# Performance work log

Hardware: AMD Instinct MI355X
Metric: run time of the kernel (lower is better)

The kernel has to match this reference:

```python
import jax, jax.numpy as jnp
import numpy as np
from jax import lax

THRESHOLD = 10.0


def _conv(x, w):
    # x: [N,1,H,W], w: [O,1,kh,kw], SAME padding, stride 1 (matches nn.Conv2d with symmetric padding)
    return lax.conv_general_dilated(x, w, window_strides=(1, 1), padding='SAME',
                                    dimension_numbers=('NCHW', 'OIHW', 'NCHW'))


def _make_filters():
    # scipy.signal.gaussian(5, std=1.0): unnormalized gaussian window
    gauss = np.exp(-0.5 * ((np.arange(5) - 2.0) ** 2)).astype(np.float32)
    gauss_w = gauss.reshape(1, 1, 1, 5)  # horizontal 1x5 filter
    sobel = np.array([[1, 0, -1], [2, 0, -2], [1, 0, -1]], np.float32)
    sobel_x = sobel[None, None]  # [1,1,3,3]
    f0 = [[0, 0, 0], [0, 1, -1], [0, 0, 0]]
    f45 = [[0, 0, 0], [0, 1, 0], [0, 0, -1]]
    f90 = [[0, 0, 0], [0, 1, 0], [0, -1, 0]]
    f135 = [[0, 0, 0], [0, 1, 0], [-1, 0, 0]]
    f180 = [[0, 0, 0], [-1, 1, 0], [0, 0, 0]]
    f225 = [[-1, 0, 0], [0, 1, 0], [0, 0, 0]]
    f270 = [[0, -1, 0], [0, 1, 0], [0, 0, 0]]
    f315 = [[0, 0, -1], [0, 1, 0], [0, 0, 0]]
    dir_w = np.stack([f0, f45, f90, f135, f180, f225, f270, f315]).astype(np.float32)[:, None]  # [8,1,3,3]
    return jnp.asarray(gauss_w), jnp.asarray(sobel_x), jnp.asarray(dir_w)


def setup_inputs() -> dict:
    key = jax.random.key(0)
    B, H, W = 4, 1024, 1024
    img = jax.random.uniform(key, (B, 3, H, W), dtype=jnp.float32) * 255.0  # pixel-scale values
    gauss_w, sobel_x, dir_w = _make_filters()
    return {'img': img, 'gauss_w': gauss_w, 'sobel_x': sobel_x, 'dir_w': dir_w}


def reference(img, gauss_w, sobel_x, dir_w):
    B, C, H, W = img.shape  # C == 3
    x = img.reshape(B * 3, 1, H, W)
    # Separable gaussian blur (horizontal then vertical), all 3 channels batched together
    blurred = _conv(_conv(x, gauss_w), jnp.transpose(gauss_w, (0, 1, 3, 2)))  # [B*3,1,H,W]
    # Sobel gradients per channel
    gx = _conv(blurred, sobel_x).reshape(B, 3, H, W)
    gy = _conv(blurred, jnp.transpose(sobel_x, (0, 1, 3, 2))).reshape(B, 3, H, W)
    # Magnitude: sum of per-channel L2 magnitudes
    grad_mag = jnp.sum(jnp.sqrt(gx * gx + gy * gy), axis=1, keepdims=True)  # [B,1,H,W]
    # Orientation from summed gradients, quantized to 45-degree bins (same pi constant as original)
    grad_orientation = jnp.arctan2(gy.sum(1, keepdims=True), gx.sum(1, keepdims=True)) * (180.0 / 3.14159)
    grad_orientation = jnp.round((grad_orientation + 180.0) / 45.0) * 45.0
    # Directional differences for non-max suppression
    all_filtered = _conv(grad_mag, dir_w)  # [B,8,H,W]
    idx_pos = ((grad_orientation / 45.0) % 8).astype(jnp.int32)          # [B,1,H,W]
    idx_neg = ((grad_orientation / 45.0 + 4.0) % 8).astype(jnp.int32)
    pos = jnp.take_along_axis(all_filtered, idx_pos, axis=1)  # [B,1,H,W]
    neg = jnp.take_along_axis(all_filtered, idx_neg, axis=1)
    is_max = jnp.minimum(pos, neg) > 0.0
    thin_edges = jnp.where(is_max, grad_mag, 0.0)
    thresholded = jnp.where(thin_edges < THRESHOLD, 0.0, thin_edges)
    early_threshold = jnp.where(grad_mag < THRESHOLD, 0.0, grad_mag)
    blurred_img = blurred.reshape(B, 3, H, W)[None]  # matches torch.stack([squeeze(...)]) for B>1
    return (blurred_img, grad_mag, grad_orientation, thin_edges, thresholded, early_threshold)
```

## Files before the change

### kernel.cpp

```cpp
#include <hip/hip_runtime.h>
#include <math.h>

#define TILE 32
#define RAW  40
#define RS   44
#define VB   36
#define MG   34
#define NT   256

struct TrigC { double c0, s0, c1, s1, c2, s2, c3, s3; };

__global__ __launch_bounds__(NT, 4) void canny_fused_kernel(
    const float* __restrict__ img,
    const float* __restrict__ gauss,
    float* __restrict__ out_blur,
    float* __restrict__ out_mag,
    float* __restrict__ out_ori,
    float* __restrict__ out_thin,
    float* __restrict__ out_thr,
    float* __restrict__ out_early,
    TrigC tc, int H, int W)
{
    __shared__ double s_raw[RAW * RS];
    __shared__ double s_vb [VB * VB];
    __shared__ double s_mag[MG * MG];

    const int tid = threadIdx.x;
    const int b   = blockIdx.z;
    const int gy0 = blockIdx.y * TILE;
    const int gx0 = blockIdx.x * TILE;
    const bool interior = (gy0 >= 4) && (gy0 + 36 <= H) && (gx0 >= 8) && (gx0 + 36 <= W);

    const double g0 = (double)gauss[0], g1 = (double)gauss[1], g2 = (double)gauss[2];
    const size_t cs = (size_t)H * W;

    for (int i = tid; i < MG * MG; i += NT) s_mag[i] = 0.0;

    double agx0 = 0.0, agx1 = 0.0, agx2 = 0.0, agx3 = 0.0;
    double agy0 = 0.0, agy1 = 0.0, agy2 = 0.0, agy3 = 0.0;

    auto load_raw = [&](int c) {
        const float* ip = img + (size_t)(b * 3 + c) * cs;
        if (interior) {
            const float* rowbase = ip + (size_t)(gy0 - 4) * W + (gx0 - 8);
            for (int t = tid; t < RAW * 11; t += NT) {
                int ry = t / 11, rx = t - ry * 11;
                float4 v = *reinterpret_cast<const float4*>(rowbase + (size_t)ry * W + rx * 4);
                double* d = &s_raw[ry * RS + rx * 4];
                d[0] = (double)v.x; d[1] = (double)v.y;
                d[2] = (double)v.z; d[3] = (double)v.w;
            }
        } else {
            for (int t = tid; t < RAW * RAW; t += NT) {
                int ry = t / RAW, rx = t - ry * RAW;
                int y = gy0 + ry - 4, x = gx0 + rx - 4;
                float v = 0.f;
                if ((unsigned)y < (unsigned)H && (unsigned)x < (unsigned)W)
                    v = ip[(size_t)y * W + x];
                s_raw[ry * RS + rx + 4] = (double)v;
            }
        }
    };

    load_raw(0);
    __syncthreads();

    for (int c = 0; c < 3; ++c) {
        if (tid < 216) {
            const int xi    = tid % 36;
            const int y0    = (tid / 36) * 6;
            const double* rb = &s_raw[xi + 4];
            auto hrow = [&](int r) -> double {
                const double* p = rb + r * RS;
                return g0 * (p[0] + p[4]) + g1 * (p[1] + p[3]) + g2 * p[2];
            };
            double h0 = hrow(y0), h1 = hrow(y0 + 1), h2 = hrow(y0 + 2),
                   h3 = hrow(y0 + 3), h4 = hrow(y0 + 4);
#pragma unroll
            for (int t = 0; t < 6; ++t) {
                int yi = y0 + t;
                double acc = g0 * (h0 + h4) + g1 * (h1 + h3) + g2 * h2;
                if (!interior) {
                    int y = gy0 + yi - 2, x = gx0 + xi - 2;
                    if ((unsigned)y >= (unsigned)H || (unsigned)x >= (unsigned)W) acc = 0.0;
                }
                s_vb[yi * VB + xi] = acc;
                if (t < 5) { h0 = h1; h1 = h2; h2 = h3; h3 = h4; h4 = hrow(yi + 5); }
            }
        }
        __syncthreads();

        {
            int ry = tid >> 5, rx = tid & 31;
#pragma unroll 4
            for (int p = 0; p < 4; ++p) {
                int my = ry + 8 * p + 1, mx = rx + 1;
                const double* v = s_vb + my * VB + mx;
                double a00 = v[0],      a01 = v[1],          a02 = v[2];
                double a10 = v[VB],                          a12 = v[VB + 2];
                double a20 = v[2 * VB], a21 = v[2 * VB + 1], a22 = v[2 * VB + 2];
                double gx = (a00 - a02) + 2.0 * (a10 - a12) + (a20 - a22);
                double gy = (a00 - a20) + 2.0 * (a01 - a21) + (a02 - a22);
                s_mag[my * MG + mx] += sqrt(gx * gx + gy * gy);
                if (p == 0) { agx0 += gx; agy0 += gy; }
                else if (p == 1) { agx1 += gx; agy1 += gy; }
                else if (p == 2) { agx2 += gx; agy2 += gy; }
                else { agx3 += gx; agy3 += gy; }
            }
        }
        if (tid < 132) {
            int my, mx;
            if (tid < 34)       { my = 0;            mx = tid; }
            else if (tid < 68)  { my = 33;           mx = tid - 34; }
            else if (tid < 100) { my = tid - 68 + 1; mx = 0; }
            else                { my = tid - 100 + 1; mx = 33; }
            bool inimg = interior;
            if (!interior) {
                int y = gy0 + my - 1, x = gx0 + mx - 1;
                inimg = ((unsigned)y < (unsigned)H) && ((unsigned)x < (unsigned)W);
            }
            if (inimg) {
                const double* v = s_vb + my * VB + mx;
                double a00 = v[0],      a01 = v[1],          a02 = v[2];
                double a10 = v[VB],                          a12 = v[VB + 2];
                double a20 = v[2 * VB], a21 = v[2 * VB + 1], a22 = v[2 * VB + 2];
                double gx = (a00 - a02) + 2.0 * (a10 - a12) + (a20 - a22);
                double gy = (a00 - a20) + 2.0 * (a01 - a21) + (a02 - a22);
                s_mag[my * MG + mx] += sqrt(gx * gx + gy * gy);
            }
        }
        {
            float* bp = out_blur + (size_t)(b * 3 + c) * cs;
            int ry = tid >> 5, rx = tid & 31;
#pragma unroll 4
            for (int p = 0; p < 4; ++p)
                bp[(size_t)(gy0 + ry + 8 * p) * W + (gx0 + rx)] =
                    (float)s_vb[(ry + 8 * p + 2) * VB + (rx + 2)];
        }
        if (c < 2) load_raw(c + 1);
        __syncthreads();
    }

    const size_t ob = (size_t)b * cs;
#pragma unroll 4
    for (int p = 0; p < 4; ++p) {
        int i = tid + p * NT;
        int ry = i >> 5, rx = i & 31;
        double gxv = (p == 0) ? agx0 : (p == 1) ? agx1 : (p == 2) ? agx2 : agx3;
        double gyv = (p == 0) ? agy0 : (p == 1) ? agy1 : (p == 2) ? agy2 : agy3;
        double m = s_mag[(ry + 1) * MG + (rx + 1)];

        double a = fabs(gyv);
        int n = (int)(a * tc.c0 - gxv * tc.s0 >= 0.0)
              + (int)(a * tc.c1 - gxv * tc.s1 >= 0.0)
              + (int)(a * tc.c2 - gxv * tc.s2 >= 0.0)
              + (int)(a * tc.c3 - gxv * tc.s3 >= 0.0);
        int k;
        if (gyv == 0.0) {
            bool gxneg = signbit(gxv);
            k = signbit(gyv) ? (gxneg ? 0 : 4) : (gxneg ? 8 : 4);
        } else {
            k = signbit(gyv) ? 4 - n : 4 + n;
        }
        float q = 45.f * (float)k;
        if (gxv < 0.0 && fabs(gyv) < 1e-2) q = 180.f;

        int kp = k & 7;
        int dy = (int)((0x00012221u >> (kp * 4)) & 7u) - 1;
        int dx = (int)((0x21000122u >> (kp * 4)) & 7u) - 1;
        double pos = m - s_mag[(ry + 1 + dy) * MG + (rx + 1 + dx)];
        double neg = m - s_mag[(ry + 1 - dy) * MG + (rx + 1 - dx)];
        float mf = (float)m;
        float thin = (fmin(pos, neg) > 0.0) ? mf : 0.f;
        size_t idx = ob + (size_t)(gy0 + ry) * W + (gx0 + rx);
        out_mag[idx]   = mf;
        out_ori[idx]   = q;
        out_thin[idx]  = thin;
        out_thr[idx]   = (thin < 10.f) ? 0.f : thin;
        out_early[idx] = (mf < 10.f) ? 0.f : mf;
    }
}

extern "C" void kernel_launch(void* const* d_in, const int* in_sizes, int n_in,
                              void* d_out, int out_size, void* d_ws, size_t ws_size,
                              hipStream_t stream) {
    const float* img   = (const float*)d_in[0];
    const float* gauss = (const float*)d_in[1];
    const int H = 1024, W = 1024;
    const int B = in_sizes[0] / (3 * H * W);

    float* out = (float*)d_out;
    const size_t cs = (size_t)H * W;
    float* out_blur  = out;
    float* out_mag   = out_blur + (size_t)B * 3 * cs;
    float* out_ori   = out_mag  + (size_t)B * cs;
    float* out_thin  = out_ori  + (size_t)B * cs;
    float* out_thr   = out_thin + (size_t)B * cs;
    float* out_early = out_thr  + (size_t)B * cs;

    const double C = 180.0 / 3.14159;
    TrigC tc;
    { double bta = 22.5 / C;  tc.c0 = cos(bta); tc.s0 = sin(bta); }
    { double bta = 67.5 / C;  tc.c1 = cos(bta); tc.s1 = sin(bta); }
    { double bta = 112.5 / C; tc.c2 = cos(bta); tc.s2 = sin(bta); }
    { double bta = 157.5 / C; tc.c3 = cos(bta); tc.s3 = sin(bta); }

    dim3 grid(W / TILE, H / TILE, B);
    canny_fused_kernel<<<grid, NT, 0, stream>>>(
        img, gauss, out_blur, out_mag, out_ori, out_thin, out_thr, out_early, tc, H, W);
}
```

Before: 80.37 us.

## Drop shared-memory raw tile and read input directly from global in blur pass

Removes the shared double-precision raw-image staging buffer and has each blur thread read its 5x10 input window straight from global memory, relying on caches for reuse. This frees about 14 KB of LDS per block, so launch bounds are raised to allow 8 blocks per CU, and one sync per channel goes away. In exchange, loads become scalar and redundant across neighbouring threads, with more global/L2 traffic and less coalescing than the float4 tile load.

Result: slower. 193.0 us (+140.2%).

```diff
diff --git a/kernel.cpp b/kernel.cpp
--- a/kernel.cpp
+++ b/kernel.cpp
@@ -2,15 +2,13 @@
 #include <math.h>
 
 #define TILE 32
-#define RAW  40
-#define RS   44
 #define VB   36
 #define MG   34
 #define NT   256
 
 struct TrigC { double c0, s0, c1, s1, c2, s2, c3, s3; };
 
-__global__ __launch_bounds__(NT, 4) void canny_fused_kernel(
+__global__ __launch_bounds__(NT, 8) void canny_fused_kernel(
     const float* __restrict__ img,
     const float* __restrict__ gauss,
     float* __restrict__ out_blur,
@@ -21,7 +19,6 @@
     float* __restrict__ out_early,
     TrigC tc, int H, int W)
 {
-    __shared__ double s_raw[RAW * RS];
     __shared__ double s_vb [VB * VB];
     __shared__ double s_mag[MG * MG];
 
@@ -29,7 +26,7 @@
     const int b   = blockIdx.z;
     const int gy0 = blockIdx.y * TILE;
     const int gx0 = blockIdx.x * TILE;
-    const bool interior = (gy0 >= 4) && (gy0 + 36 <= H) && (gx0 >= 8) && (gx0 + 36 <= W);
+    const bool interior = (gy0 >= 4) && (gy0 + 36 <= H) && (gx0 >= 4) && (gx0 + 36 <= W);
 
     const double g0 = (double)gauss[0], g1 = (double)gauss[1], g2 = (double)gauss[2];
     const size_t cs = (size_t)H * W;
@@ -39,53 +36,52 @@
     double agx0 = 0.0, agx1 = 0.0, agx2 = 0.0, agx3 = 0.0;
     double agy0 = 0.0, agy1 = 0.0, agy2 = 0.0, agy3 = 0.0;
 
-    auto load_raw = [&](int c) {
-        const float* ip = img + (size_t)(b * 3 + c) * cs;
-        if (interior) {
-            const float* rowbase = ip + (size_t)(gy0 - 4) * W + (gx0 - 8);
-            for (int t = tid; t < RAW * 11; t += NT) {
-                int ry = t / 11, rx = t - ry * 11;
-                float4 v = *reinterpret_cast<const float4*>(rowbase + (size_t)ry * W + rx * 4);
-                double* d = &s_raw[ry * RS + rx * 4];
-                d[0] = (double)v.x; d[1] = (double)v.y;
-                d[2] = (double)v.z; d[3] = (double)v.w;
-            }
-        } else {
-            for (int t = tid; t < RAW * RAW; t += NT) {
-                int ry = t / RAW, rx = t - ry * RAW;
-                int y = gy0 + ry - 4, x = gx0 + rx - 4;
-                float v = 0.f;
-                if ((unsigned)y < (unsigned)H && (unsigned)x < (unsigned)W)
-                    v = ip[(size_t)y * W + x];
-                s_raw[ry * RS + rx + 4] = (double)v;
-            }
-        }
-    };
-
-    load_raw(0);
-    __syncthreads();
-
     for (int c = 0; c < 3; ++c) {
         if (tid < 216) {
-            const int xi    = tid % 36;
-            const int y0    = (tid / 36) * 6;
-            const double* rb = &s_raw[xi + 4];
-            auto hrow = [&](int r) -> double {
-                const double* p = rb + r * RS;
-                return g0 * (p[0] + p[4]) + g1 * (p[1] + p[3]) + g2 * p[2];
-            };
-            double h0 = hrow(y0), h1 = hrow(y0 + 1), h2 = hrow(y0 + 2),
-                   h3 = hrow(y0 + 3), h4 = hrow(y0 + 4);
+            const int xi = tid % 36;
+            const int y0 = (tid / 36) * 6;
+            const float* ip = img + (size_t)(b * 3 + c) * cs;
+            const int xb = gx0 + xi - 4;
+            const int gy = gy0 + y0 - 4;
+            if (interior) {
+                const float* colp = ip + xb;
+                auto hrow = [&](int yy) -> double {
+                    const float* p = colp + (size_t)yy * W;
+                    return g0 * ((double)p[0] + (double)p[4])
+                         + g1 * ((double)p[1] + (double)p[3])
+                         + g2 * (double)p[2];
+                };
+                double h0 = hrow(gy),     h1 = hrow(gy + 1), h2 = hrow(gy + 2),
+                       h3 = hrow(gy + 3), h4 = hrow(gy + 4);
 #pragma unroll
-            for (int t = 0; t < 6; ++t) {
-                int yi = y0 + t;
-                double acc = g0 * (h0 + h4) + g1 * (h1 + h3) + g2 * h2;
-                if (!interior) {
+                for (int t = 0; t < 6; ++t) {
+                    s_vb[(y0 + t) * VB + xi] = g0 * (h0 + h4) + g1 * (h1 + h3) + g2 * h2;
+                    if (t < 5) { h0 = h1; h1 = h2; h2 = h3; h3 = h4; h4 = hrow(gy + 5 + t); }
+                }
+            } else {
+                auto hrow = [&](int yy) -> double {
+                    if ((unsigned)yy >= (unsigned)H) return 0.0;
+                    const float* p = ip + (size_t)yy * W;
+                    double s = 0.0;
+                    int x;
+                    x = xb;     if ((unsigned)x < (unsigned)W) s += g0 * (double)p[x];
+                    x = xb + 1; if ((unsigned)x < (unsigned)W) s += g1 * (double)p[x];
+                    x = xb + 2; if ((unsigned)x < (unsigned)W) s += g2 * (double)p[x];
+                    x = xb + 3; if ((unsigned)x < (unsigned)W) s += g1 * (double)p[x];
+                    x = xb + 4; if ((unsigned)x < (unsigned)W) s += g0 * (double)p[x];
+                    return s;
+                };
+                double h0 = hrow(gy),     h1 = hrow(gy + 1), h2 = hrow(gy + 2),
+                       h3 = hrow(gy + 3), h4 = hrow(gy + 4);
+#pragma unroll
+                for (int t = 0; t < 6; ++t) {
+                    int yi = y0 + t;
+                    double acc = g0 * (h0 + h4) + g1 * (h1 + h3) + g2 * h2;
                     int y = gy0 + yi - 2, x = gx0 + xi - 2;
                     if ((unsigned)y >= (unsigned)H || (unsigned)x >= (unsigned)W) acc = 0.0;
+                    s_vb[yi * VB + xi] = acc;
+                    if (t < 5) { h0 = h1; h1 = h2; h2 = h3; h3 = h4; h4 = hrow(gy + 5 + t); }
                 }
-                s_vb[yi * VB + xi] = acc;
-                if (t < 5) { h0 = h1; h1 = h2; h2 = h3; h3 = h4; h4 = hrow(yi + 5); }
             }
         }
         __syncthreads();
@@ -110,9 +106,9 @@
         }
         if (tid < 132) {
             int my, mx;
-            if (tid < 34)       { my = 0;            mx = tid; }
-            else if (tid < 68)  { my = 33;           mx = tid - 34; }
-            else if (tid < 100) { my = tid - 68 + 1; mx = 0; }
+            if (tid < 34)       { my = 0;             mx = tid; }
+            else if (tid < 68)  { my = 33;            mx = tid - 34; }
+            else if (tid < 100) { my = tid - 68 + 1;  mx = 0; }
             else                { my = tid - 100 + 1; mx = 33; }
             bool inimg = interior;
             if (!interior) {
@@ -137,7 +133,6 @@
                 bp[(size_t)(gy0 + ry + 8 * p) * W + (gx0 + rx)] =
                     (float)s_vb[(ry + 8 * p + 2) * VB + (rx + 2)];
         }
-        if (c < 2) load_raw(c + 1);
         __syncthreads();
     }
 
```
